# Kernel optimization log

Measured on AMD Instinct MI355X. Metric: run time of the kernel, lower is better.

Reference implementation:

```python
import jax, jax.numpy as jnp
import numpy as np

D = 32        # number of causal nodes
DF = 256      # d * factor (factor=8)
BATCH = 32768


def setup_inputs() -> dict:
    key = jax.random.key(0)
    ks = jax.random.split(key, 16)
    f32 = jnp.float32

    def w(k, shape, fan_in):
        return (jax.random.normal(k, shape, f32) / np.sqrt(fan_in)).astype(f32)

    return {
        "xor": jax.random.normal(ks[0], (BATCH, D), f32),
        "m": jax.random.normal(ks[1], (BATCH, D), f32),   # unused by the module
        "eps": jax.random.normal(ks[2], (BATCH, D), f32),  # reparameterization noise
        # encoder: enc1 (d->df), enc2 (df->df, 1 extra layer), enc3 (df->2d)
        "We1": w(ks[3], (D, DF), D),   "be1": jnp.zeros((DF,), f32),
        "We2": w(ks[4], (DF, DF), DF), "be2": jnp.zeros((DF,), f32),
        "We3": w(ks[5], (DF, 2 * D), DF), "be3": jnp.zeros((2 * D,), f32),
        # per-node decoder stacks. dec1[i] is Linear(i+1 -> DF); we store it as a
        # full [D, DF] weight per node and mask the inputs (columns > i are masked
        # to zero before the matmul), which is mathematically identical to the
        # ragged gather + small Linear in the original.
        "W1": w(ks[6], (D, D, DF), D),  "b1": jnp.zeros((D, DF), f32),
        "W2": w(ks[7], (D, DF, DF), DF), "b2": jnp.zeros((D, DF), f32),
        "W3": w(ks[8], (D, DF), DF),     "b3": jnp.zeros((D,), f32),
    }


def reference(xor, m, eps, We1, be1, We2, be2, We3, be3, W1, b1, W2, b2, W3, b3):
    d = W1.shape[0]
    # encoder: relu(enc1) -> [Linear->ReLU] -> enc3 -> view(-1, 2, d)
    h = jax.nn.relu(xor @ We1 + be1)
    h = jax.nn.relu(h @ We2 + be2)
    z = (h @ We3 + be3).reshape(-1, 2, d)
    mu = z[:, 0, :]
    log_var = z[:, 1, :]
    y0 = mu + jnp.exp(log_var / 2) * eps  # rsample

    node_idx = jnp.arange(d)

    # sequential decode: node i reads columns B[:, i] = {0..i} of the CURRENT
    # y_recon (earlier nodes already overwritten), then overwrites column i.
    def body(y, i):
        mask = (node_idx <= i).astype(y.dtype)          # parents 0..i-1 plus self
        t = jax.nn.relu((y * mask) @ W1[i] + b1[i])     # [B, DF]
        t = jax.nn.relu(t @ W2[i] + b2[i])              # [B, DF]
        out = t @ W3[i] + b3[i]                         # [B]
        y = y.at[:, i].set(out)
        return y, None

    y, _ = jax.lax.scan(body, y0, jnp.arange(d))
    # no_noise=True: x[:, i] = y_recon[:, i], so x == final y_recon
    return (y, mu, log_var, y)
```

## Files before the change

kernel.cpp:

```cpp
#include <hip/hip_runtime.h>

#define DD 32
#define DFF 256
#define BATCH_N 32768
#define ROWS 64
#define THREADS 256
#define BD (BATCH_N * DD)
#define YPITCH 40
#define YFP 33

typedef __bf16 bf16x8 __attribute__((ext_vector_type(8)));
typedef __bf16 bf16x4 __attribute__((ext_vector_type(4)));
typedef float f32x4 __attribute__((ext_vector_type(4)));

__device__ __forceinline__ unsigned short f2bf(float f) {
  unsigned int u = __builtin_bit_cast(unsigned int, f);
  u += 0x7FFFu + ((u >> 16) & 1u);
  return (unsigned short)(u >> 16);
}

__global__ void repack_kernel(const float* __restrict__ src,
                              unsigned short* __restrict__ dst,
                              int K, int N, long sstride, long dstride) {
  long mat = blockIdx.y;
  int p = blockIdx.x * 256 + threadIdx.x;
  if (p >= K * N) return;
  int NT = N >> 4;
  int j = p & 7;
  int l = (p >> 3) & 63;
  int rest = p >> 9;
  int nt = rest % NT;
  int ks = rest / NT;
  int k = ks * 32 + ((l >> 4) << 3) + j;
  int n = nt * 16 + (l & 15);
  dst[mat * dstride + p] = f2bf(src[mat * sstride + (long)k * N + n]);
}

__device__ __forceinline__ int swzA(int row, int col) {
  return ((row * DFF + col) * 2) ^ ((row & 7) << 4);
}
__device__ __forceinline__ bf16x8 ldA(const unsigned short* buf, int row, int k0) {
  return __builtin_bit_cast(bf16x8, *(const uint4*)((const char*)buf + swzA(row, k0)));
}
__device__ __forceinline__ bf16x8 ldY(const unsigned short* ybf, int row, int k0) {
  return __builtin_bit_cast(bf16x8, *(const uint4*)(ybf + row * YPITCH + k0));
}
__device__ __forceinline__ uint4 ldWraw(const unsigned short* __restrict__ wp,
                                        int ks, int NT, int ntAbs, int lane) {
  return *(const uint4*)(wp + ((((ks * NT + ntAbs) << 6) + lane) << 3));
}
__device__ __forceinline__ bf16x8 asw(uint4 v) { return __builtin_bit_cast(bf16x8, v); }

#define MFMA16(a, b, c) __builtin_amdgcn_mfma_f32_16x16x32_bf16((a), (b), (c), 0, 0, 0)

__device__ __forceinline__ void biasInit(f32x4 acc[4][4], const float* __restrict__ b,
                                         int ng, int lg) {
#pragma unroll
  for (int nt = 0; nt < 4; ++nt) {
    f32x4 bv = *(const f32x4*)(b + (ng * 4 + nt) * 16 + lg * 4);
#pragma unroll
    for (int rt = 0; rt < 4; ++rt) acc[nt][rt] = bv;
  }
}

__device__ __forceinline__ void storeAct(unsigned short* act, f32x4 acc[4][4],
                                         int ng, int lr, int lg) {
#pragma unroll
  for (int nt = 0; nt < 4; ++nt) {
    int n = (ng * 4 + nt) * 16 + lg * 4;
#pragma unroll
    for (int rt = 0; rt < 4; ++rt) {
      int r = rt * 16 + lr;
      bf16x4 w;
#pragma unroll
      for (int rr = 0; rr < 4; ++rr) w[rr] = (__bf16)fmaxf(acc[nt][rt][rr], 0.f);
      *(bf16x4*)((char*)act + swzA(r, n)) = w;
    }
  }
}

__global__ __launch_bounds__(THREADS, 2)
void vae_kernel(const float* __restrict__ xin, const float* __restrict__ eps,
                const float* __restrict__ be1, const float* __restrict__ be2,
                const float* __restrict__ be3, const float* __restrict__ b1,
                const float* __restrict__ b2, const float* __restrict__ W3,
                const float* __restrict__ b3,
                const unsigned short* __restrict__ We1p,
                const unsigned short* __restrict__ We2p,
                const unsigned short* __restrict__ We3p,
                const unsigned short* __restrict__ W1p,
                const unsigned short* __restrict__ W2p,
                float* __restrict__ out) {
  __shared__ __align__(16) unsigned short act[ROWS * DFF];
  __shared__ unsigned short ybf[ROWS * YPITCH];
  __shared__ float yf[ROWS * YFP];
  __shared__ float red[4 * ROWS];

  const int tid = threadIdx.x;
  const int lane = tid & 63;
  const int ng = tid >> 6;
  const int lr = lane & 15;
  const int lg = lane >> 4;
  const long r0 = (long)blockIdx.x * ROWS;

  for (int e = tid; e < ROWS * DD; e += THREADS) {
    int rr = e >> 5, d = e & 31;
    ybf[rr * YPITCH + d] = f2bf(xin[(r0 + rr) * DD + d]);
  }
  __syncthreads();

  f32x4 acc[4][4];

  biasInit(acc, be1, ng, lg);
  {
    bf16x8 yb[4];
#pragma unroll
    for (int rt = 0; rt < 4; ++rt) yb[rt] = ldY(ybf, rt * 16 + lr, lg * 8);
#pragma unroll
    for (int nt = 0; nt < 4; ++nt) {
      bf16x8 w = asw(ldWraw(We1p, 0, 16, ng * 4 + nt, lane));
#pragma unroll
      for (int rt = 0; rt < 4; ++rt) acc[nt][rt] = MFMA16(w, yb[rt], acc[nt][rt]);
    }
  }
  storeAct(act, acc, ng, lr, lg);
  __syncthreads();

  biasInit(acc, be2, ng, lg);
#pragma unroll
  for (int ks = 0; ks < 8; ++ks) {
    bf16x8 ab[4];
#pragma unroll
    for (int rt = 0; rt < 4; ++rt) ab[rt] = ldA(act, rt * 16 + lr, ks * 32 + lg * 8);
#pragma unroll
    for (int nt = 0; nt < 4; ++nt) {
      bf16x8 w = asw(ldWraw(We2p, ks, 16, ng * 4 + nt, lane));
#pragma unroll
      for (int rt = 0; rt < 4; ++rt) acc[nt][rt] = MFMA16(w, ab[rt], acc[nt][rt]);
    }
  }
  __syncthreads();
  storeAct(act, acc, ng, lr, lg);
  __syncthreads();

  {
    f32x4 az[4];
    f32x4 bz = *(const f32x4*)(be3 + ng * 16 + lg * 4);
#pragma unroll
    for (int rt = 0; rt < 4; ++rt) az[rt] = bz;
#pragma unroll
    for (int ks = 0; ks < 8; ++ks) {
      bf16x8 w = asw(ldWraw(We3p, ks, 4, ng, lane));
#pragma unroll
      for (int rt = 0; rt < 4; ++rt) {
        bf16x8 a = ldA(act, rt * 16 + lr, ks * 32 + lg * 8);
        az[rt] = MFMA16(w, a, az[rt]);
      }
    }
    __syncthreads();
    float* zt = (float*)act;
#pragma unroll
    for (int rt = 0; rt < 4; ++rt) {
      int r = rt * 16 + lr;
#pragma unroll
      for (int rr = 0; rr < 4; ++rr)
        zt[(ng * 16 + lg * 4 + rr) * 66 + r] = az[rt][rr];
    }
  }
  __syncthreads();

  {
    const float* zt = (const float*)act;
    for (int e = tid; e < ROWS * DD; e += THREADS) {
      int rr = e >> 5, d = e & 31;
      float mu = zt[d * 66 + rr];
      float lv = zt[(32 + d) * 66 + rr];
      long gi = (r0 + rr) * DD + d;
      float y0 = mu + __expf(0.5f * lv) * eps[gi];
      yf[rr * YFP + d] = y0;
      ybf[rr * YPITCH + d] = (d == 0) ? f2bf(y0) : (unsigned short)0;
      out[BD + gi] = mu;
      out[2L * BD + gi] = lv;
    }
  }

  uint4 w1f[4], w2f[4][4];
#pragma unroll
  for (int nt = 0; nt < 4; ++nt) w1f[nt] = ldWraw(W1p, 0, 16, ng * 4 + nt, lane);
#pragma unroll
  for (int ks = 0; ks < 4; ++ks)
#pragma unroll
    for (int nt = 0; nt < 4; ++nt) w2f[ks][nt] = ldWraw(W2p, ks, 16, ng * 4 + nt, lane);
  __syncthreads();

#pragma unroll 1
  for (int i = 0; i < DD; ++i) {
    const unsigned short* W2cur = W2p + i * (DFF * DFF);
    const int inx = (i + 1 < DD) ? i + 1 : i;
    const unsigned short* W1nx = W1p + inx * (DD * DFF);
    const unsigned short* W2nx = W2p + inx * (DFF * DFF);

    biasInit(acc, b1 + i * DFF, ng, lg);
    {
      bf16x8 yb[4];
#pragma unroll
      for (int rt = 0; rt < 4; ++rt) yb[rt] = ldY(ybf, rt * 16 + lr, lg * 8);
#pragma unroll
      for (int nt = 0; nt < 4; ++nt) {
        bf16x8 w = asw(w1f[nt]);
#pragma unroll
        for (int rt = 0; rt < 4; ++rt) acc[nt][rt] = MFMA16(w, yb[rt], acc[nt][rt]);
      }
    }
    storeAct(act, acc, ng, lr, lg);
    __syncthreads();

    biasInit(acc, b2 + i * DFF, ng, lg);
#pragma unroll
    for (int ks = 0; ks < 4; ++ks) {
      bf16x8 ab[4];
#pragma unroll
      for (int rt = 0; rt < 4; ++rt) ab[rt] = ldA(act, rt * 16 + lr, ks * 32 + lg * 8);
#pragma unroll
      for (int nt = 0; nt < 4; ++nt) {
        bf16x8 w = asw(w2f[ks][nt]);
#pragma unroll
        for (int rt = 0; rt < 4; ++rt) acc[nt][rt] = MFMA16(w, ab[rt], acc[nt][rt]);
        w2f[ks][nt] = ldWraw(W2cur, ks + 4, 16, ng * 4 + nt, lane);
      }
    }
#pragma unroll
    for (int ks = 4; ks < 8; ++ks) {
      bf16x8 ab[4];
#pragma unroll
      for (int rt = 0; rt < 4; ++rt) ab[rt] = ldA(act, rt * 16 + lr, ks * 32 + lg * 8);
#pragma unroll
      for (int nt = 0; nt < 4; ++nt) {
        bf16x8 w = asw(w2f[ks - 4][nt]);
#pragma unroll
        for (int rt = 0; rt < 4; ++rt) acc[nt][rt] = MFMA16(w, ab[rt], acc[nt][rt]);
        w2f[ks - 4][nt] = ldWraw(W2nx, ks - 4, 16, ng * 4 + nt, lane);
      }
    }
#pragma unroll
    for (int nt = 0; nt < 4; ++nt) w1f[nt] = ldWraw(W1nx, 0, 16, ng * 4 + nt, lane);

    const float* w3r = W3 + i * DFF;
    float part[4] = {0.f, 0.f, 0.f, 0.f};
#pragma unroll
    for (int nt = 0; nt < 4; ++nt) {
      f32x4 w3v = *(const f32x4*)(w3r + (ng * 4 + nt) * 16 + lg * 4);
#pragma unroll
      for (int rt = 0; rt < 4; ++rt)
#pragma unroll
        for (int rr = 0; rr < 4; ++rr)
          part[rt] = fmaf(fmaxf(acc[nt][rt][rr], 0.f), w3v[rr], part[rt]);
    }
#pragma unroll
    for (int rt = 0; rt < 4; ++rt) {
      part[rt] += __shfl_xor(part[rt], 16);
      part[rt] += __shfl_xor(part[rt], 32);
    }
    if (lg == 0) {
#pragma unroll
      for (int rt = 0; rt < 4; ++rt) red[ng * ROWS + rt * 16 + lr] = part[rt];
    }
    __syncthreads();

    if (tid < ROWS) {
      float v = b3[i] + red[tid] + red[ROWS + tid] + red[2 * ROWS + tid] + red[3 * ROWS + tid];
      yf[tid * YFP + i] = v;
      ybf[tid * YPITCH + i] = f2bf(v);
      if (i + 1 < DD)
        ybf[tid * YPITCH + i + 1] = f2bf(yf[tid * YFP + i + 1]);
    }
    __syncthreads();
  }

  for (int e = tid; e < ROWS * DD; e += THREADS) {
    int rr = e >> 5, d = e & 31;
    long gi = (r0 + rr) * DD + d;
    float v = yf[rr * YFP + d];
    out[gi] = v;
    out[3L * BD + gi] = v;
  }
}

extern "C" void kernel_launch(void* const* d_in, const int* in_sizes, int n_in,
                              void* d_out, int out_size, void* d_ws, size_t ws_size,
                              hipStream_t stream) {
  const float* xin = (const float*)d_in[0];
  const float* eps = (const float*)d_in[2];
  const float* We1 = (const float*)d_in[3];
  const float* be1 = (const float*)d_in[4];
  const float* We2 = (const float*)d_in[5];
  const float* be2 = (const float*)d_in[6];
  const float* We3 = (const float*)d_in[7];
  const float* be3 = (const float*)d_in[8];
  const float* W1  = (const float*)d_in[9];
  const float* b1  = (const float*)d_in[10];
  const float* W2  = (const float*)d_in[11];
  const float* b2  = (const float*)d_in[12];
  const float* W3  = (const float*)d_in[13];
  const float* b3  = (const float*)d_in[14];
  float* out = (float*)d_out;

  unsigned short* We1p = (unsigned short*)d_ws;
  unsigned short* We2p = We1p + 32 * 256;
  unsigned short* We3p = We2p + 256 * 256;
  unsigned short* W1p  = We3p + 256 * 64;
  unsigned short* W2p  = W1p + 32 * 32 * 256;

  repack_kernel<<<dim3(32, 1), 256, 0, stream>>>(We1, We1p, 32, 256, 0, 0);
  repack_kernel<<<dim3(256, 1), 256, 0, stream>>>(We2, We2p, 256, 256, 0, 0);
  repack_kernel<<<dim3(64, 1), 256, 0, stream>>>(We3, We3p, 256, 64, 0, 0);
  repack_kernel<<<dim3(32, 32), 256, 0, stream>>>(W1, W1p, 32, 256, 32 * 256, 32 * 256);
  repack_kernel<<<dim3(256, 32), 256, 0, stream>>>(W2, W2p, 256, 256, 256 * 256, 256 * 256);

  vae_kernel<<<dim3(BATCH_N / ROWS), THREADS, 0, stream>>>(
      xin, eps, be1, be2, be3, b1, b2, W3, b3, We1p, We2p, We3p, W1p, W2p, out);
}
```

Baseline: 212.7 us.

## Keep decoder y state in registers and drop per-step barrier

```diff
diff --git a/kernel.cpp b/kernel.cpp
--- a/kernel.cpp
+++ b/kernel.cpp
@@ -6,8 +6,8 @@
 #define ROWS 64
 #define THREADS 256
 #define BD (BATCH_N * DD)
-#define YPITCH 40
-#define YFP 33
+#define Y0P 40
+#define ZTP 66
 
 typedef __bf16 bf16x8 __attribute__((ext_vector_type(8)));
 typedef __bf16 bf16x4 __attribute__((ext_vector_type(4)));
@@ -42,8 +42,8 @@
 __device__ __forceinline__ bf16x8 ldA(const unsigned short* buf, int row, int k0) {
   return __builtin_bit_cast(bf16x8, *(const uint4*)((const char*)buf + swzA(row, k0)));
 }
-__device__ __forceinline__ bf16x8 ldY(const unsigned short* ybf, int row, int k0) {
-  return __builtin_bit_cast(bf16x8, *(const uint4*)(ybf + row * YPITCH + k0));
+__device__ __forceinline__ bf16x8 ldY0(const unsigned short* y0b, int row, int k0) {
+  return __builtin_bit_cast(bf16x8, *(const uint4*)(y0b + row * Y0P + k0));
 }
 __device__ __forceinline__ uint4 ldWraw(const unsigned short* __restrict__ wp,
                                         int ks, int NT, int ntAbs, int lane) {
@@ -92,8 +92,7 @@
                 const unsigned short* __restrict__ W2p,
                 float* __restrict__ out) {
   __shared__ __align__(16) unsigned short act[ROWS * DFF];
-  __shared__ unsigned short ybf[ROWS * YPITCH];
-  __shared__ float yf[ROWS * YFP];
+  __shared__ __align__(16) unsigned short y0b[ROWS * Y0P];
   __shared__ float red[4 * ROWS];
 
   const int tid = threadIdx.x;
@@ -105,7 +104,7 @@
 
   for (int e = tid; e < ROWS * DD; e += THREADS) {
     int rr = e >> 5, d = e & 31;
-    ybf[rr * YPITCH + d] = f2bf(xin[(r0 + rr) * DD + d]);
+    y0b[rr * Y0P + d] = f2bf(xin[(r0 + rr) * DD + d]);
   }
   __syncthreads();
 
@@ -115,7 +114,7 @@
   {
     bf16x8 yb[4];
 #pragma unroll
-    for (int rt = 0; rt < 4; ++rt) yb[rt] = ldY(ybf, rt * 16 + lr, lg * 8);
+    for (int rt = 0; rt < 4; ++rt) yb[rt] = ldY0(y0b, rt * 16 + lr, lg * 8);
 #pragma unroll
     for (int nt = 0; nt < 4; ++nt) {
       bf16x8 w = asw(ldWraw(We1p, 0, 16, ng * 4 + nt, lane));
@@ -164,7 +163,7 @@
       int r = rt * 16 + lr;
 #pragma unroll
       for (int rr = 0; rr < 4; ++rr)
-        zt[(ng * 16 + lg * 4 + rr) * 66 + r] = az[rt][rr];
+        zt[(ng * 16 + lg * 4 + rr) * ZTP + r] = az[rt][rr];
     }
   }
   __syncthreads();
@@ -173,12 +172,11 @@
     const float* zt = (const float*)act;
     for (int e = tid; e < ROWS * DD; e += THREADS) {
       int rr = e >> 5, d = e & 31;
-      float mu = zt[d * 66 + rr];
-      float lv = zt[(32 + d) * 66 + rr];
+      float mu = zt[d * ZTP + rr];
+      float lv = zt[(32 + d) * ZTP + rr];
       long gi = (r0 + rr) * DD + d;
       float y0 = mu + __expf(0.5f * lv) * eps[gi];
-      yf[rr * YFP + d] = y0;
-      ybf[rr * YPITCH + d] = (d == 0) ? f2bf(y0) : (unsigned short)0;
+      y0b[rr * Y0P + d] = f2bf(y0);
       out[BD + gi] = mu;
       out[2L * BD + gi] = lv;
     }
@@ -193,96 +191,117 @@
     for (int nt = 0; nt < 4; ++nt) w2f[ks][nt] = ldWraw(W2p, ks, 16, ng * 4 + nt, lane);
   __syncthreads();
 
+  bf16x8 yreg[4];
+#pragma unroll
+  for (int rt = 0; rt < 4; ++rt) {
+    uint4 z4 = {0u, 0u, 0u, 0u};
+    yreg[rt] = asw(z4);
+  }
+  if (lg == 0) {
+#pragma unroll
+    for (int rt = 0; rt < 4; ++rt)
+      yreg[rt][0] = __builtin_bit_cast(__bf16, y0b[(rt * 16 + lr) * Y0P]);
+  }
+
 #pragma unroll 1
-  for (int i = 0; i < DD; ++i) {
-    const unsigned short* W2cur = W2p + i * (DFF * DFF);
-    const int inx = (i + 1 < DD) ? i + 1 : i;
-    const unsigned short* W1nx = W1p + inx * (DD * DFF);
-    const unsigned short* W2nx = W2p + inx * (DFF * DFF);
-
-    biasInit(acc, b1 + i * DFF, ng, lg);
-    {
-      bf16x8 yb[4];
-#pragma unroll
-      for (int rt = 0; rt < 4; ++rt) yb[rt] = ldY(ybf, rt * 16 + lr, lg * 8);
+  for (int i8 = 0; i8 < 4; ++i8) {
+#pragma unroll
+    for (int u = 0; u < 8; ++u) {
+      const int i = i8 * 8 + u;
+      const unsigned short* W2cur = W2p + i * (DFF * DFF);
+      const int inx = (i + 1 < DD) ? i + 1 : DD - 1;
+      const unsigned short* W1nx = W1p + inx * (DD * DFF);
+      const unsigned short* W2nx = W2p + inx * (DFF * DFF);
+      const float b3i = b3[i];
+
+      biasInit(acc, b1 + i * DFF, ng, lg);
 #pragma unroll
       for (int nt = 0; nt < 4; ++nt) {
         bf16x8 w = asw(w1f[nt]);
 #pragma unroll
-        for (int rt = 0; rt < 4; ++rt) acc[nt][rt] = MFMA16(w, yb[rt], acc[nt][rt]);
-      }
-    }
-    storeAct(act, acc, ng, lr, lg);
-    __syncthreads();
-
-    biasInit(acc, b2 + i * DFF, ng, lg);
-#pragma unroll
-    for (int ks = 0; ks < 4; ++ks) {
-      bf16x8 ab[4];
-#pragma unroll
-      for (int rt = 0; rt < 4; ++rt) ab[rt] = ldA(act, rt * 16 + lr, ks * 32 + lg * 8);
+        for (int rt = 0; rt < 4; ++rt) acc[nt][rt] = MFMA16(w, yreg[rt], acc[nt][rt]);
+      }
+      storeAct(act, acc, ng, lr, lg);
+      __syncthreads();
+
+      biasInit(acc, b2 + i * DFF, ng, lg);
+      __builtin_amdgcn_s_setprio(1);
+#pragma unroll
+      for (int ks = 0; ks < 4; ++ks) {
+        bf16x8 ab[4];
+#pragma unroll
+        for (int rt = 0; rt < 4; ++rt) ab[rt] = ldA(act, rt * 16 + lr, ks * 32 + lg * 8);
+#pragma unroll
+        for (int nt = 0; nt < 4; ++nt) {
+          bf16x8 w = asw(w2f[ks][nt]);
+#pragma unroll
+          for (int rt = 0; rt < 4; ++rt) acc[nt][rt] = MFMA16(w, ab[rt], acc[nt][rt]);
+          w2f[ks][nt] = ldWraw(W2cur, ks + 4, 16, ng * 4 + nt, lane);
+        }
+      }
+#pragma unroll
+      for (int ks = 4; ks < 8; ++ks) {
+        bf16x8 ab[4];
+#pragma unroll
+        for (int rt = 0; rt < 4; ++rt) ab[rt] = ldA(act, rt * 16 + lr, ks * 32 + lg * 8);
+#pragma unroll
+        for (int nt = 0; nt < 4; ++nt) {
+          bf16x8 w = asw(w2f[ks - 4][nt]);
+#pragma unroll
+          for (int rt = 0; rt < 4; ++rt) acc[nt][rt] = MFMA16(w, ab[rt], acc[nt][rt]);
+          w2f[ks - 4][nt] = ldWraw(W2nx, ks - 4, 16, ng * 4 + nt, lane);
+        }
+      }
+      __builtin_amdgcn_s_setprio(0);
+#pragma unroll
+      for (int nt = 0; nt < 4; ++nt) w1f[nt] = ldWraw(W1nx, 0, 16, ng * 4 + nt, lane);
+
+      const float* w3r = W3 + i * DFF;
+      float part[4] = {0.f, 0.f, 0.f, 0.f};
 #pragma unroll
       for (int nt = 0; nt < 4; ++nt) {
-        bf16x8 w = asw(w2f[ks][nt]);
-#pragma unroll
-        for (int rt = 0; rt < 4; ++rt) acc[nt][rt] = MFMA16(w, ab[rt], acc[nt][rt]);
-        w2f[ks][nt] = ldWraw(W2cur, ks + 4, 16, ng * 4 + nt, lane);
-      }
-    }
-#pragma unroll
-    for (int ks = 4; ks < 8; ++ks) {
-      bf16x8 ab[4];
-#pragma unroll
-      for (int rt = 0; rt < 4; ++rt) ab[rt] = ldA(act, rt * 16 + lr, ks * 32 + lg * 8);
-#pragma unroll
-      for (int nt = 0; nt < 4; ++nt) {
-        bf16x8 w = asw(w2f[ks - 4][nt]);
-#pragma unroll
-        for (int rt = 0; rt < 4; ++rt) acc[nt][rt] = MFMA16(w, ab[rt], acc[nt][rt]);
-        w2f[ks - 4][nt] = ldWraw(W2nx, ks - 4, 16, ng * 4 + nt, lane);
-      }
-    }
-#pragma unroll
-    for (int nt = 0; nt < 4; ++nt) w1f[nt] = ldWraw(W1nx, 0, 16, ng * 4 + nt, lane);
-
-    const float* w3r = W3 + i * DFF;
-    float part[4] = {0.f, 0.f, 0.f, 0.f};
-#pragma unroll
-    for (int nt = 0; nt < 4; ++nt) {
-      f32x4 w3v = *(const f32x4*)(w3r + (ng * 4 + nt) * 16 + lg * 4);
-#pragma unroll
-      for (int rt = 0; rt < 4; ++rt)
-#pragma unroll
-        for (int rr = 0; rr < 4; ++rr)
-          part[rt] = fmaf(fmaxf(acc[nt][rt][rr], 0.f), w3v[rr], part[rt]);
-    }
-#pragma unroll
-    for (int rt = 0; rt < 4; ++rt) {
-      part[rt] += __shfl_xor(part[rt], 16);
-      part[rt] += __shfl_xor(part[rt], 32);
-    }
-    if (lg == 0) {
-#pragma unroll
-      for (int rt = 0; rt < 4; ++rt) red[ng * ROWS + rt * 16 + lr] = part[rt];
-    }
-    __syncthreads();
-
-    if (tid < ROWS) {
-      float v = b3[i] + red[tid] + red[ROWS + tid] + red[2 * ROWS + tid] + red[3 * ROWS + tid];
-      yf[tid * YFP + i] = v;
-      ybf[tid * YPITCH + i] = f2bf(v);
-      if (i + 1 < DD)
-        ybf[tid * YPITCH + i + 1] = f2bf(yf[tid * YFP + i + 1]);
-    }
-    __syncthreads();
-  }
-
-  for (int e = tid; e < ROWS * DD; e += THREADS) {
-    int rr = e >> 5, d = e & 31;
-    long gi = (r0 + rr) * DD + d;
-    float v = yf[rr * YFP + d];
-    out[gi] = v;
-    out[3L * BD + gi] = v;
+        f32x4 w3v = *(const f32x4*)(w3r + (ng * 4 + nt) * 16 + lg * 4);
+#pragma unroll
+        for (int rt = 0; rt < 4; ++rt)
+#pragma unroll
+          for (int rr = 0; rr < 4; ++rr)
+            part[rt] = fmaf(fmaxf(acc[nt][rt][rr], 0.f), w3v[rr], part[rt]);
+      }
+#pragma unroll
+      for (int rt = 0; rt < 4; ++rt) {
+        part[rt] += __shfl_xor(part[rt], 16);
+        part[rt] += __shfl_xor(part[rt], 32);
+      }
+      if (lg == 0) {
+#pragma unroll
+        for (int rt = 0; rt < 4; ++rt) red[ng * ROWS + rt * 16 + lr] = part[rt];
+      }
+      __syncthreads();
+
+      if (tid < ROWS) {
+        float v = b3i + red[tid] + red[ROWS + tid] + red[2 * ROWS + tid] + red[3 * ROWS + tid];
+        long gi = (r0 + tid) * DD + i;
+        out[gi] = v;
+        out[3L * BD + gi] = v;
+      }
+      if (lg == i8) {
+#pragma unroll
+        for (int rt = 0; rt < 4; ++rt) {
+          int row = rt * 16 + lr;
+          float v = b3i + red[row] + red[ROWS + row] + red[2 * ROWS + row] + red[3 * ROWS + row];
+          yreg[rt][u] = __builtin_bit_cast(__bf16, f2bf(v));
+        }
+      }
+      if (i + 1 < DD) {
+        const int lg2 = (i + 1) >> 3;
+        if (lg == lg2) {
+#pragma unroll
+          for (int rt = 0; rt < 4; ++rt)
+            yreg[rt][(u + 1) & 7] =
+                __builtin_bit_cast(__bf16, y0b[(rt * 16 + lr) * Y0P + i + 1]);
+        }
+      }
+    }
   }
 }
 
```

Result: slower. 234.0 us (+10.0%).
